# Performance work log

Measured on AMD Instinct MI355X. Metric: run time of the kernel, lower is better.

The kernel has to match this reference:

```python
import jax, jax.numpy as jnp
import numpy as np

N_NODES = 100000
N_EDGES = 600000
HID = 128
N_ETYPES = 8


def setup_inputs() -> dict:
    key = jax.random.key(0)
    ks = jax.random.split(key, 10)
    s = 1.0 / np.sqrt(HID)
    return {
        "h": jax.random.normal(ks[0], (N_NODES, HID), dtype=jnp.float32),
        "edge_index": jax.random.randint(ks[1], (2, N_EDGES), 0, N_NODES, dtype=jnp.int64),
        "edge_type": jax.random.randint(ks[2], (N_EDGES,), 0, N_ETYPES, dtype=jnp.int64),
        # per-edge-type Linear(hidden, hidden): weight (T, H_out, H_in) stored as (T, H_in, H_out) for einsum
        "message_W": jax.random.uniform(ks[3], (N_ETYPES, HID, HID), jnp.float32, -s, s),
        "message_b": jax.random.uniform(ks[4], (N_ETYPES, HID), jnp.float32, -s, s),
        # GRUCell params (torch layout): w_ih (3H, H), w_hh (3H, H), b_ih (3H,), b_hh (3H,)
        "gru_w_ih": jax.random.uniform(ks[5], (3 * HID, HID), jnp.float32, -s, s),
        "gru_w_hh": jax.random.uniform(ks[6], (3 * HID, HID), jnp.float32, -s, s),
        "gru_b_ih": jax.random.uniform(ks[7], (3 * HID,), jnp.float32, -s, s),
        "gru_b_hh": jax.random.uniform(ks[8], (3 * HID,), jnp.float32, -s, s),
    }


def reference(h, edge_index, edge_type, message_W, message_b,
              gru_w_ih, gru_w_hh, gru_b_ih, gru_b_hh):
    num_nodes = h.shape[0]
    src, dst = edge_index[0], edge_index[1]

    # Transform every node by every edge-type Linear once: (N, T, H).
    # Equivalent to per-type msg = h[src] @ W[t].T + b[t] gathered by edge type.
    all_msgs = jnp.einsum('nh,thd->ntd', h, message_W) + message_b  # (N, T, H)
    msg = all_msgs[src, edge_type]                                   # (E, H) gather
    messages = jax.ops.segment_sum(msg, dst, num_segments=num_nodes)  # scatter-add

    # GRUCell: r,z,n gates (torch semantics)
    gi = messages @ gru_w_ih.T + gru_b_ih  # (N, 3H)
    gh = h @ gru_w_hh.T + gru_b_hh         # (N, 3H)
    i_r, i_z, i_n = jnp.split(gi, 3, axis=-1)
    h_r, h_z, h_n = jnp.split(gh, 3, axis=-1)
    r = jax.nn.sigmoid(i_r + h_r)
    z = jax.nn.sigmoid(i_z + h_z)
    n = jnp.tanh(i_n + r * h_n)
    return (1.0 - z) * n + z * h
```

## Files before the change

### kernel.cpp

```cpp
#include <hip/hip_runtime.h>

#define HID 128
#define NTY 8

typedef __attribute__((ext_vector_type(8))) short bf16x8;
typedef __attribute__((ext_vector_type(4))) float f32x4;

__device__ __forceinline__ unsigned short f2bf(float x) {
    unsigned u = __float_as_uint(x);
    u += 0x7FFF + ((u >> 16) & 1);
    return (unsigned short)(u >> 16);
}
__device__ __forceinline__ float bf2f(unsigned short s) {
    return __uint_as_float(((unsigned)s) << 16);
}
__device__ __forceinline__ float sigmoidf_fast(float x) {
    return 1.f / (1.f + __expf(-x));
}
__device__ __forceinline__ float tanhf_fast(float x) {
    return 1.f - 2.f / (1.f + __expf(2.f * x));
}

__global__ void conv_h_kernel(const float* __restrict__ h, unsigned short* __restrict__ hbf, int n) {
    int i = blockIdx.x * 256 + threadIdx.x;
    if (i < n) hbf[i] = f2bf(h[i]);
}
__global__ void conv_W_kernel(const float* __restrict__ W, unsigned short* __restrict__ WbfT) {
    int i = blockIdx.x * 256 + threadIdx.x;
    int t = i >> 14, rem = i & 16383, d = rem >> 7, k = rem & 127;
    WbfT[(t << 14) + (d << 7) + k] = f2bf(W[(t << 14) + (k << 7) + d]);
}
__global__ void conv_wpk_kernel(const float* __restrict__ wih, const float* __restrict__ whh,
                                unsigned short* __restrict__ wpk) {
    int i = blockIdx.x * 256 + threadIdx.x;
    if (i >= 8 * 3 * 128 * 32) return;
    int kk = i & 31;
    int rest = i >> 5;
    int d = rest & 127;
    int rest2 = rest >> 7;
    int g3 = rest2 % 3, kc = rest2 / 3;
    float v;
    if (kc < 4) v = wih[(g3 * 128 + d) * 128 + kc * 32 + kk];
    else        v = whh[(g3 * 128 + d) * 128 + (kc - 4) * 32 + kk];
    wpk[i] = f2bf(v);
}

__global__ void hist_kernel(const int* __restrict__ etype, const int* __restrict__ ei,
                            int E, int* __restrict__ tcnt, int* __restrict__ deg) {
    __shared__ int lc[NTY];
    if (threadIdx.x < NTY) lc[threadIdx.x] = 0;
    __syncthreads();
    int stride = gridDim.x * blockDim.x;
    for (int i = blockIdx.x * blockDim.x + threadIdx.x; i < E; i += stride) {
        atomicAdd(&lc[etype[i]], 1);
        if (deg) atomicAdd(&deg[ei[E + i]], 1);
    }
    __syncthreads();
    if (threadIdx.x < NTY) atomicAdd(&tcnt[threadIdx.x], lc[threadIdx.x]);
}

__global__ void scan_type_kernel(const int* __restrict__ tcnt, int* __restrict__ tcur) {
    if (threadIdx.x == 0) {
        int off = 0;
        for (int t = 0; t < NTY; ++t) { tcur[t] = off; off += (tcnt[t] + 127) & ~127; }
    }
}

__global__ void scanA_kernel(const int* __restrict__ deg, int* __restrict__ start,
                             int* __restrict__ bsum, int N) {
    __shared__ int s[256];
    int i = blockIdx.x * 256 + threadIdx.x;
    int v = (i < N) ? deg[i] : 0;
    s[threadIdx.x] = v;
    __syncthreads();
    for (int off = 1; off < 256; off <<= 1) {
        int t = (threadIdx.x >= off) ? s[threadIdx.x - off] : 0;
        __syncthreads();
        s[threadIdx.x] += t;
        __syncthreads();
    }
    if (i < N) start[i] = s[threadIdx.x] - v;
    if (threadIdx.x == 255) bsum[blockIdx.x] = s[255];
}

__global__ void scanB_kernel(int* __restrict__ bsum, int nb) {
    __shared__ int s[512];
    int tx = threadIdx.x;
    int v = (tx < nb) ? bsum[tx] : 0;
    s[tx] = v;
    __syncthreads();
    for (int off = 1; off < 512; off <<= 1) {
        int t = (tx >= off) ? s[tx - off] : 0;
        __syncthreads();
        s[tx] += t;
        __syncthreads();
    }
    if (tx < nb) bsum[tx] = s[tx] - v;
}

__global__ void scanC_kernel(int* __restrict__ start, const int* __restrict__ bsum,
                             int* __restrict__ dcur, int N, int E) {
    int i = blockIdx.x * 256 + threadIdx.x;
    if (i < N) {
        int v = start[i] + bsum[blockIdx.x];
        start[i] = v;
        dcur[i] = v;
    }
    if (i == 0) start[N] = E;
}

__global__ __launch_bounds__(256) void scatter_agg(
    const int* __restrict__ etype, const int* __restrict__ ei, int E,
    int* __restrict__ tcur, int* __restrict__ dcur,
    int* __restrict__ sortedT, int* __restrict__ q, int mode)
{
    __shared__ int lcnt[NTY];
    __shared__ int lbase[NTY];
    int tx = threadIdx.x;
    int chunk = (E + gridDim.x - 1) / gridDim.x;
    int s = blockIdx.x * chunk;
    int e = s + chunk; if (e > E) e = E;
    if (tx < NTY) lcnt[tx] = 0;
    __syncthreads();
    for (int i = s + tx; i < e; i += 256)
        atomicAdd(&lcnt[etype[i]], 1);
    __syncthreads();
    if (tx < NTY) {
        lbase[tx] = atomicAdd(&tcur[tx], lcnt[tx]);
        lcnt[tx] = 0;
    }
    __syncthreads();
    for (int i = s + tx; i < e; i += 256) {
        int t = etype[i];
        int lp = atomicAdd(&lcnt[t], 1);
        sortedT[lbase[t] + lp] = i;
        if (mode) q[i] = atomicAdd(&dcur[ei[E + i]], 1);
    }
}

__global__ __launch_bounds__(256) void msg_gemm(
    const unsigned short* __restrict__ hbf, const int* __restrict__ ei, int E,
    const int* __restrict__ etype, const unsigned short* __restrict__ WbfT,
    const float* __restrict__ bias, const int* __restrict__ sortedT,
    const int* __restrict__ q, unsigned short* __restrict__ M,
    float* __restrict__ msum, int mode)
{
    __shared__ unsigned short hs[128][136];
    __shared__ unsigned short Bs[128][40];
    __shared__ int srcs[128], aux[128];
    __shared__ int stype;

    int tx = threadIdx.x;
    int base = blockIdx.x * 128;
    if (tx < 128) {
        int id = sortedT[base + tx];
        srcs[tx] = (id >= 0) ? ei[id] : -1;
        aux[tx]  = (id >= 0) ? (mode ? ei[E + id] : q[id]) : -1;
    }
    if (tx == 0) { int id0 = sortedT[base]; stype = (id0 >= 0) ? etype[id0] : -1; }
    __syncthreads();
    int t = stype;
    if (t < 0) return;

    const unsigned short* Wb = WbfT + (t << 14);

    for (int f = tx; f < 2048; f += 256) {
        int row = f >> 4, c8 = (f & 15) * 8;
        int s = srcs[row]; if (s < 0) s = 0;
        *(uint4*)&hs[row][c8] = *(const uint4*)&hbf[(size_t)s * 128 + c8];
    }

    int lane = tx & 63, w = tx >> 6;
    int r0 = (w >> 1) * 64, c0 = (w & 1) * 64;
    int lr = lane & 15, quad = lane >> 4;
    f32x4 acc[4][4] = {};

    for (int kc = 0; kc < 4; ++kc) {
        __syncthreads();
        for (int f = tx; f < 512; f += 256) {
            int d = f >> 2, c8 = (f & 3) * 8;
            *(uint4*)&Bs[d][c8] = *(const uint4*)&Wb[(d << 7) + kc * 32 + c8];
        }
        __syncthreads();
        bf16x8 af[4], bfr[4];
        #pragma unroll
        for (int rb = 0; rb < 4; ++rb) af[rb]  = *(const bf16x8*)&hs[r0 + rb * 16 + lr][kc * 32 + quad * 8];
        #pragma unroll
        for (int cb = 0; cb < 4; ++cb) bfr[cb] = *(const bf16x8*)&Bs[c0 + cb * 16 + lr][quad * 8];
        #pragma unroll
        for (int rb = 0; rb < 4; ++rb)
            #pragma unroll
            for (int cb = 0; cb < 4; ++cb)
                acc[rb][cb] = __builtin_amdgcn_mfma_f32_16x16x32_bf16(bfr[cb], af[rb], acc[rb][cb], 0, 0, 0);
    }

    float4 bv4[4];
    #pragma unroll
    for (int cb = 0; cb < 4; ++cb)
        bv4[cb] = *(const float4*)&bias[t * 128 + c0 + cb * 16 + quad * 4];

    #pragma unroll
    for (int rb = 0; rb < 4; ++rb) {
        int e = r0 + rb * 16 + lr;
        int mr = aux[e];
        if (mr < 0) continue;
        #pragma unroll
        for (int cb = 0; cb < 4; ++cb) {
            int d0 = c0 + cb * 16 + quad * 4;
            f32x4 a = acc[rb][cb];
            if (mode) {
                atomicAdd(&msum[(size_t)mr * 128 + d0 + 0], a[0] + bv4[cb].x);
                atomicAdd(&msum[(size_t)mr * 128 + d0 + 1], a[1] + bv4[cb].y);
                atomicAdd(&msum[(size_t)mr * 128 + d0 + 2], a[2] + bv4[cb].z);
                atomicAdd(&msum[(size_t)mr * 128 + d0 + 3], a[3] + bv4[cb].w);
            } else {
                uint2 v;
                v.x = (unsigned)f2bf(a[0] + bv4[cb].x) | ((unsigned)f2bf(a[1] + bv4[cb].y) << 16);
                v.y = (unsigned)f2bf(a[2] + bv4[cb].z) | ((unsigned)f2bf(a[3] + bv4[cb].w) << 16);
                *(uint2*)&M[(size_t)mr * 128 + d0] = v;
            }
        }
    }
}

__global__ __launch_bounds__(256) void gru_fused(
    const unsigned short* __restrict__ M, const int* __restrict__ start,
    const float* __restrict__ msum_fb, const unsigned short* __restrict__ hbf,
    const unsigned short* __restrict__ wpk, const float* __restrict__ bih,
    const float* __restrict__ bhh, const float* __restrict__ hf,
    float* __restrict__ out, int N, int mode)
{
    __shared__ unsigned short As[64][264];

    int tx = threadIdx.x;
    int n0 = blockIdx.x * 64;

    {
        int node = tx >> 2, qd = tx & 3;
        int n = n0 + node;
        int nc = (n < N) ? n : N - 1;
        float a[32];
        #pragma unroll
        for (int j = 0; j < 32; ++j) a[j] = 0.f;
        if (mode == 0) {
            int s = start[nc], e = start[nc + 1];
            for (int r = s; r < e; ++r) {
                #pragma unroll
                for (int j = 0; j < 4; ++j) {
                    uint4 v = *(const uint4*)&M[(size_t)r * 128 + qd * 32 + j * 8];
                    const unsigned short* pv = (const unsigned short*)&v;
                    #pragma unroll
                    for (int u = 0; u < 8; ++u) a[j * 8 + u] += bf2f(pv[u]);
                }
            }
        } else {
            #pragma unroll
            for (int j = 0; j < 8; ++j) {
                float4 v = *(const float4*)&msum_fb[(size_t)nc * 128 + qd * 32 + j * 4];
                a[j * 4 + 0] = v.x; a[j * 4 + 1] = v.y; a[j * 4 + 2] = v.z; a[j * 4 + 3] = v.w;
            }
        }
        unsigned short tmp[32];
        #pragma unroll
        for (int j = 0; j < 32; ++j) tmp[j] = f2bf(a[j]);
        #pragma unroll
        for (int j = 0; j < 4; ++j)
            *(uint4*)&As[node][qd * 32 + j * 8] = *(const uint4*)&tmp[j * 8];
        #pragma unroll
        for (int j = 0; j < 4; ++j)
            *(uint4*)&As[node][128 + qd * 32 + j * 8] =
                *(const uint4*)&hbf[(size_t)nc * 128 + qd * 32 + j * 8];
    }
    __syncthreads();

    int lane = tx & 63, w = tx >> 6;
    int rt = w & 1, cg = w >> 1;
    int lr = lane & 15, quad = lane >> 4;

    f32x4 aR[4][2] = {}, aZ[4][2] = {}, aI[4][2] = {}, aH[4][2] = {};

    #pragma unroll
    for (int kc = 0; kc < 4; ++kc) {
        bf16x8 af[2];
        #pragma unroll
        for (int r2 = 0; r2 < 2; ++r2)
            af[r2] = *(const bf16x8*)&As[rt * 32 + r2 * 16 + lr][kc * 32 + quad * 8];
        #pragma unroll
        for (int g3 = 0; g3 < 3; ++g3) {
            #pragma unroll
            for (int ct = 0; ct < 4; ++ct) {
                bf16x8 bf = *(const bf16x8*)&wpk[((size_t)((kc * 3 + g3) * 128) + cg * 64 + ct * 16 + lr) * 32 + quad * 8];
                #pragma unroll
                for (int r2 = 0; r2 < 2; ++r2) {
                    if (g3 == 0) aR[ct][r2] = __builtin_amdgcn_mfma_f32_16x16x32_bf16(bf, af[r2], aR[ct][r2], 0, 0, 0);
                    else if (g3 == 1) aZ[ct][r2] = __builtin_amdgcn_mfma_f32_16x16x32_bf16(bf, af[r2], aZ[ct][r2], 0, 0, 0);
                    else aI[ct][r2] = __builtin_amdgcn_mfma_f32_16x16x32_bf16(bf, af[r2], aI[ct][r2], 0, 0, 0);
                }
            }
        }
    }
    #pragma unroll
    for (int kc = 4; kc < 8; ++kc) {
        bf16x8 af[2];
        #pragma unroll
        for (int r2 = 0; r2 < 2; ++r2)
            af[r2] = *(const bf16x8*)&As[rt * 32 + r2 * 16 + lr][kc * 32 + quad * 8];
        #pragma unroll
        for (int g3 = 0; g3 < 3; ++g3) {
            #pragma unroll
            for (int ct = 0; ct < 4; ++ct) {
                bf16x8 bf = *(const bf16x8*)&wpk[((size_t)((kc * 3 + g3) * 128) + cg * 64 + ct * 16 + lr) * 32 + quad * 8];
                #pragma unroll
                for (int r2 = 0; r2 < 2; ++r2) {
                    if (g3 == 0) aR[ct][r2] = __builtin_amdgcn_mfma_f32_16x16x32_bf16(bf, af[r2], aR[ct][r2], 0, 0, 0);
                    else if (g3 == 1) aZ[ct][r2] = __builtin_amdgcn_mfma_f32_16x16x32_bf16(bf, af[r2], aZ[ct][r2], 0, 0, 0);
                    else aH[ct][r2] = __builtin_amdgcn_mfma_f32_16x16x32_bf16(bf, af[r2], aH[ct][r2], 0, 0, 0);
                }
            }
        }
    }

    #pragma unroll
    for (int ct = 0; ct < 4; ++ct) {
        int d0 = cg * 64 + ct * 16 + quad * 4;
        f32x4 bi_r = *(const f32x4*)&bih[d0];
        f32x4 bh_r = *(const f32x4*)&bhh[d0];
        f32x4 bi_z = *(const f32x4*)&bih[128 + d0];
        f32x4 bh_z = *(const f32x4*)&bhh[128 + d0];
        f32x4 bi_n = *(const f32x4*)&bih[256 + d0];
        f32x4 bh_n = *(const f32x4*)&bhh[256 + d0];
        #pragma unroll
        for (int r2 = 0; r2 < 2; ++r2) {
            int n = n0 + rt * 32 + r2 * 16 + lr;
            if (n >= N) continue;
            f32x4 h0 = *(const f32x4*)&hf[(size_t)n * 128 + d0];
            f32x4 o;
            #pragma unroll
            for (int j = 0; j < 4; ++j) {
                float r  = sigmoidf_fast(aR[ct][r2][j] + bi_r[j] + bh_r[j]);
                float z  = sigmoidf_fast(aZ[ct][r2][j] + bi_z[j] + bh_z[j]);
                float nn = tanhf_fast(aI[ct][r2][j] + bi_n[j] + r * (aH[ct][r2][j] + bh_n[j]));
                o[j] = (1.f - z) * nn + z * h0[j];
            }
            *(f32x4*)&out[(size_t)n * 128 + d0] = o;
        }
    }
}

extern "C" void kernel_launch(void* const* d_in, const int* in_sizes, int n_in,
                              void* d_out, int out_size, void* d_ws, size_t ws_size,
                              hipStream_t stream)
{
    const float* h     = (const float*)d_in[0];
    const int*   ei    = (const int*)d_in[1];
    const int*   etype = (const int*)d_in[2];
    const float* W     = (const float*)d_in[3];
    const float* b     = (const float*)d_in[4];
    const float* wih   = (const float*)d_in[5];
    const float* whh   = (const float*)d_in[6];
    const float* bih   = (const float*)d_in[7];
    const float* bhh   = (const float*)d_in[8];
    float* out = (float*)d_out;

    int E = in_sizes[1] / 2;
    int N = in_sizes[0] / HID;
    int capE = ((E + 127) / 128 + NTY) * 128;

    char* p = (char*)d_ws;
    auto alloc = [&](size_t bytes) { char* r = p; p += (bytes + 255) & ~(size_t)255; return r; };
    unsigned short* hbf  = (unsigned short*)alloc((size_t)N * 128 * 2);
    unsigned short* WbfT = (unsigned short*)alloc((size_t)8 * 128 * 128 * 2);
    unsigned short* wpk  = (unsigned short*)alloc((size_t)8 * 3 * 128 * 32 * 2);
    int* tcnt    = (int*)alloc(NTY * 4);
    int* tcur    = (int*)alloc(NTY * 4);
    int* sortedT = (int*)alloc((size_t)capE * 4);
    unsigned short* M = (unsigned short*)alloc((size_t)E * 128 * 2);
    int* q     = (int*)alloc((size_t)E * 4);
    int* deg   = (int*)alloc((size_t)N * 4);
    int* start = (int*)alloc((size_t)(N + 1) * 4);
    int* dcur  = (int*)alloc((size_t)N * 4);
    int* bsum  = (int*)alloc(512 * 4);
    int mode = ((size_t)(p - (char*)d_ws) <= ws_size) ? 0 : 1;

    hipMemsetAsync(tcnt, 0, NTY * 4, stream);
    hipMemsetAsync(sortedT, 0xFF, (size_t)capE * 4, stream);
    if (mode == 0) hipMemsetAsync(deg, 0, (size_t)N * 4, stream);
    else           hipMemsetAsync(out, 0, (size_t)N * 128 * 4, stream);

    conv_h_kernel<<<(N * 128 + 255) / 256, 256, 0, stream>>>(h, hbf, N * 128);
    conv_W_kernel<<<(8 * 128 * 128) / 256, 256, 0, stream>>>(W, WbfT);
    conv_wpk_kernel<<<(8 * 3 * 128 * 32 + 255) / 256, 256, 0, stream>>>(wih, whh, wpk);

    hist_kernel<<<1024, 256, 0, stream>>>(etype, ei, E, tcnt, (mode == 0) ? deg : nullptr);
    scan_type_kernel<<<1, 64, 0, stream>>>(tcnt, tcur);
    if (mode == 0) {
        int nbA = (N + 255) / 256;
        scanA_kernel<<<nbA, 256, 0, stream>>>(deg, start, bsum, N);
        scanB_kernel<<<1, 512, 0, stream>>>(bsum, nbA);
        scanC_kernel<<<nbA, 256, 0, stream>>>(start, bsum, dcur, N, E);
    }
    scatter_agg<<<256, 256, 0, stream>>>(etype, ei, E, tcur, dcur, sortedT, q, (mode == 0) ? 1 : 0);

    msg_gemm<<<capE / 128, 256, 0, stream>>>(hbf, ei, E, etype, WbfT, b, sortedT, q, M, out, mode);
    gru_fused<<<(N + 63) / 64, 256, 0, stream>>>(M, start, out, hbf, wpk, bih, bhh, h, out, N, mode);
}
```

Baseline: 411.7 us.

## Fuse prep kernels, prepack weights in MFMA fragment order, restructure GRU GEMM

Merges the three conversion kernels and the memsets into one launch, and folds the type scan into scanB, cutting launch count. Weights are prepacked in MFMA fragment order, so msg_gemm and gru_fused read B fragments straight from global memory without LDS staging or per-k syncthreads. gru_fused now gives each wave its own 16 nodes, loads h fragments straight into registers, and uses a swizzled per-wave LDS tile. It also splits the work into two output halves to reduce accumulator pressure. The M-row gather loop is software-prefetched one row ahead. The cost is more global and L2 weight traffic per wave and more register use.

```diff
diff --git a/kernel.cpp b/kernel.cpp
--- a/kernel.cpp
+++ b/kernel.cpp
@@ -21,28 +21,44 @@
     return 1.f - 2.f / (1.f + __expf(2.f * x));
 }
 
-__global__ void conv_h_kernel(const float* __restrict__ h, unsigned short* __restrict__ hbf, int n) {
+__global__ void conv_all_kernel(const float* __restrict__ h, unsigned short* __restrict__ hbf, int nh,
+                                const float* __restrict__ W, unsigned short* __restrict__ wfr,
+                                const float* __restrict__ wih, const float* __restrict__ whh,
+                                unsigned short* __restrict__ wpkf,
+                                int* __restrict__ sortedT, int capE,
+                                int* __restrict__ deg, int N, int* __restrict__ tcnt)
+{
     int i = blockIdx.x * 256 + threadIdx.x;
-    if (i < n) hbf[i] = f2bf(h[i]);
-}
-__global__ void conv_W_kernel(const float* __restrict__ W, unsigned short* __restrict__ WbfT) {
-    int i = blockIdx.x * 256 + threadIdx.x;
-    int t = i >> 14, rem = i & 16383, d = rem >> 7, k = rem & 127;
-    WbfT[(t << 14) + (d << 7) + k] = f2bf(W[(t << 14) + (k << 7) + d]);
-}
-__global__ void conv_wpk_kernel(const float* __restrict__ wih, const float* __restrict__ whh,
-                                unsigned short* __restrict__ wpk) {
-    int i = blockIdx.x * 256 + threadIdx.x;
-    if (i >= 8 * 3 * 128 * 32) return;
-    int kk = i & 31;
-    int rest = i >> 5;
-    int d = rest & 127;
-    int rest2 = rest >> 7;
-    int g3 = rest2 % 3, kc = rest2 / 3;
-    float v;
-    if (kc < 4) v = wih[(g3 * 128 + d) * 128 + kc * 32 + kk];
-    else        v = whh[(g3 * 128 + d) * 128 + (kc - 4) * 32 + kk];
-    wpk[i] = f2bf(v);
+    if (i < nh) { hbf[i] = f2bf(h[i]); return; }
+    i -= nh;
+    if (i < 131072) {
+        int e = i & 7, lane = (i >> 3) & 63, cb = (i >> 9) & 7, kc = (i >> 12) & 3, t = i >> 14;
+        int lr = lane & 15, quad = lane >> 4;
+        int d = cb * 16 + lr;
+        int k = kc * 32 + quad * 8 + e;
+        wfr[i] = f2bf(W[(t << 14) + (k << 7) + d]);
+        return;
+    }
+    i -= 131072;
+    if (i < 98304) {
+        int e = i & 7, lane = (i >> 3) & 63, f = i >> 9;
+        int ct = f & 7, fg = f >> 3;
+        int g3 = fg % 3, kc = fg / 3;
+        int lr = lane & 15, quad = lane >> 4;
+        int d = ct * 16 + lr;
+        int kk = quad * 8 + e;
+        float v;
+        if (kc < 4) v = wih[(g3 * 128 + d) * 128 + kc * 32 + kk];
+        else        v = whh[(g3 * 128 + d) * 128 + (kc - 4) * 32 + kk];
+        wpkf[i] = f2bf(v);
+        return;
+    }
+    i -= 98304;
+    if (i < capE) { sortedT[i] = -1; return; }
+    i -= capE;
+    if (i < N) { deg[i] = 0; return; }
+    i -= N;
+    if (i < NTY) tcnt[i] = 0;
 }
 
 __global__ void hist_kernel(const int* __restrict__ etype, const int* __restrict__ ei,
@@ -57,13 +73,6 @@
     }
     __syncthreads();
     if (threadIdx.x < NTY) atomicAdd(&tcnt[threadIdx.x], lc[threadIdx.x]);
-}
-
-__global__ void scan_type_kernel(const int* __restrict__ tcnt, int* __restrict__ tcur) {
-    if (threadIdx.x == 0) {
-        int off = 0;
-        for (int t = 0; t < NTY; ++t) { tcur[t] = off; off += (tcnt[t] + 127) & ~127; }
-    }
 }
 
 __global__ void scanA_kernel(const int* __restrict__ deg, int* __restrict__ start,
@@ -83,7 +92,8 @@
     if (threadIdx.x == 255) bsum[blockIdx.x] = s[255];
 }
 
-__global__ void scanB_kernel(int* __restrict__ bsum, int nb) {
+__global__ void scanB_kernel(int* __restrict__ bsum, int nb,
+                             const int* __restrict__ tcnt, int* __restrict__ tcur) {
     __shared__ int s[512];
     int tx = threadIdx.x;
     int v = (tx < nb) ? bsum[tx] : 0;
@@ -96,6 +106,10 @@
         __syncthreads();
     }
     if (tx < nb) bsum[tx] = s[tx] - v;
+    if (tx == 0) {
+        int off = 0;
+        for (int t = 0; t < NTY; ++t) { tcur[t] = off; off += (tcnt[t] + 127) & ~127; }
+    }
 }
 
 __global__ void scanC_kernel(int* __restrict__ start, const int* __restrict__ bsum,
@@ -140,13 +154,12 @@
 
 __global__ __launch_bounds__(256) void msg_gemm(
     const unsigned short* __restrict__ hbf, const int* __restrict__ ei, int E,
-    const int* __restrict__ etype, const unsigned short* __restrict__ WbfT,
+    const int* __restrict__ etype, const unsigned short* __restrict__ wfr,
     const float* __restrict__ bias, const int* __restrict__ sortedT,
     const int* __restrict__ q, unsigned short* __restrict__ M,
     float* __restrict__ msum, int mode)
 {
     __shared__ unsigned short hs[128][136];
-    __shared__ unsigned short Bs[128][40];
     __shared__ int srcs[128], aux[128];
     __shared__ int stype;
 
@@ -162,36 +175,31 @@
     int t = stype;
     if (t < 0) return;
 
-    const unsigned short* Wb = WbfT + (t << 14);
-
     for (int f = tx; f < 2048; f += 256) {
         int row = f >> 4, c8 = (f & 15) * 8;
         int s = srcs[row]; if (s < 0) s = 0;
         *(uint4*)&hs[row][c8] = *(const uint4*)&hbf[(size_t)s * 128 + c8];
     }
+    __syncthreads();
 
     int lane = tx & 63, w = tx >> 6;
     int r0 = (w >> 1) * 64, c0 = (w & 1) * 64;
     int lr = lane & 15, quad = lane >> 4;
     f32x4 acc[4][4] = {};
 
+    const unsigned short* wt = wfr + (t << 14) + ((unsigned)(c0 >> 4) << 9) + (lane << 3);
+    #pragma unroll
     for (int kc = 0; kc < 4; ++kc) {
-        __syncthreads();
-        for (int f = tx; f < 512; f += 256) {
-            int d = f >> 2, c8 = (f & 3) * 8;
-            *(uint4*)&Bs[d][c8] = *(const uint4*)&Wb[(d << 7) + kc * 32 + c8];
-        }
-        __syncthreads();
-        bf16x8 af[4], bfr[4];
-        #pragma unroll
-        for (int rb = 0; rb < 4; ++rb) af[rb]  = *(const bf16x8*)&hs[r0 + rb * 16 + lr][kc * 32 + quad * 8];
-        #pragma unroll
-        for (int cb = 0; cb < 4; ++cb) bfr[cb] = *(const bf16x8*)&Bs[c0 + cb * 16 + lr][quad * 8];
+        bf16x8 af[4], wf[4];
+        #pragma unroll
+        for (int rb = 0; rb < 4; ++rb) af[rb] = *(const bf16x8*)&hs[r0 + rb * 16 + lr][kc * 32 + quad * 8];
+        #pragma unroll
+        for (int cb = 0; cb < 4; ++cb) wf[cb] = *(const bf16x8*)&wt[(kc << 12) + (cb << 9)];
         #pragma unroll
         for (int rb = 0; rb < 4; ++rb)
             #pragma unroll
             for (int cb = 0; cb < 4; ++cb)
-                acc[rb][cb] = __builtin_amdgcn_mfma_f32_16x16x32_bf16(bfr[cb], af[rb], acc[rb][cb], 0, 0, 0);
+                acc[rb][cb] = __builtin_amdgcn_mfma_f32_16x16x32_bf16(wf[cb], af[rb], acc[rb][cb], 0, 0, 0);
     }
 
     float4 bv4[4];
@@ -226,11 +234,11 @@
 __global__ __launch_bounds__(256) void gru_fused(
     const unsigned short* __restrict__ M, const int* __restrict__ start,
     const float* __restrict__ msum_fb, const unsigned short* __restrict__ hbf,
-    const unsigned short* __restrict__ wpk, const float* __restrict__ bih,
+    const unsigned short* __restrict__ wpkf, const float* __restrict__ bih,
     const float* __restrict__ bhh, const float* __restrict__ hf,
     float* __restrict__ out, int N, int mode)
 {
-    __shared__ unsigned short As[64][264];
+    __shared__ unsigned short As[4][2048];
 
     int tx = threadIdx.x;
     int n0 = blockIdx.x * 64;
@@ -244,13 +252,33 @@
         for (int j = 0; j < 32; ++j) a[j] = 0.f;
         if (mode == 0) {
             int s = start[nc], e = start[nc + 1];
+            uint4 c0v, c1v, c2v, c3v;
+            if (s < e) {
+                const unsigned short* Mp = M + (size_t)s * 128 + qd * 32;
+                c0v = *(const uint4*)(Mp);
+                c1v = *(const uint4*)(Mp + 8);
+                c2v = *(const uint4*)(Mp + 16);
+                c3v = *(const uint4*)(Mp + 24);
+            }
             for (int r = s; r < e; ++r) {
+                uint4 p0 = c0v, p1 = c1v, p2 = c2v, p3 = c3v;
+                if (r + 1 < e) {
+                    const unsigned short* Mn = M + (size_t)(r + 1) * 128 + qd * 32;
+                    c0v = *(const uint4*)(Mn);
+                    c1v = *(const uint4*)(Mn + 8);
+                    c2v = *(const uint4*)(Mn + 16);
+                    c3v = *(const uint4*)(Mn + 24);
+                }
+                const unsigned short* q0 = (const unsigned short*)&p0;
+                const unsigned short* q1 = (const unsigned short*)&p1;
+                const unsigned short* q2 = (const unsigned short*)&p2;
+                const unsigned short* q3 = (const unsigned short*)&p3;
                 #pragma unroll
-                for (int j = 0; j < 4; ++j) {
-                    uint4 v = *(const uint4*)&M[(size_t)r * 128 + qd * 32 + j * 8];
-                    const unsigned short* pv = (const unsigned short*)&v;
-                    #pragma unroll
-                    for (int u = 0; u < 8; ++u) a[j * 8 + u] += bf2f(pv[u]);
+                for (int u = 0; u < 8; ++u) {
+                    a[u]      += bf2f(q0[u]);
+                    a[8 + u]  += bf2f(q1[u]);
+                    a[16 + u] += bf2f(q2[u]);
+                    a[24 + u] += bf2f(q3[u]);
                 }
             }
         } else {
@@ -263,86 +291,93 @@
         unsigned short tmp[32];
         #pragma unroll
         for (int j = 0; j < 32; ++j) tmp[j] = f2bf(a[j]);
-        #pragma unroll
-        for (int j = 0; j < 4; ++j)
-            *(uint4*)&As[node][qd * 32 + j * 8] = *(const uint4*)&tmp[j * 8];
-        #pragma unroll
-        for (int j = 0; j < 4; ++j)
-            *(uint4*)&As[node][128 + qd * 32 + j * 8] =
-                *(const uint4*)&hbf[(size_t)nc * 128 + qd * 32 + j * 8];
+        int lrw = node & 15, wv = node >> 4;
+        #pragma unroll
+        for (int j = 0; j < 4; ++j) {
+            int byte = (lrw << 8) + (qd << 6) + (j << 4);
+            byte ^= (lrw & 7) << 4;
+            *(uint4*)((char*)&As[wv][0] + byte) = *(const uint4*)&tmp[j * 8];
+        }
     }
     __syncthreads();
 
     int lane = tx & 63, w = tx >> 6;
-    int rt = w & 1, cg = w >> 1;
     int lr = lane & 15, quad = lane >> 4;
-
-    f32x4 aR[4][2] = {}, aZ[4][2] = {}, aI[4][2] = {}, aH[4][2] = {};
+    int node = n0 + w * 16 + lr;
+    bool valid = node < N;
+    int nc = valid ? node : (N - 1);
+    unsigned short* AsW = &As[w][0];
+
+    bf16x8 afh[4];
+    {
+        const unsigned short* hrow = hbf + ((size_t)nc << 7) + (quad << 3);
+        #pragma unroll
+        for (int k4 = 0; k4 < 4; ++k4) afh[k4] = *(const bf16x8*)&hrow[k4 * 32];
+    }
+    const unsigned short* wg = wpkf + (lane << 3);
 
     #pragma unroll
-    for (int kc = 0; kc < 4; ++kc) {
-        bf16x8 af[2];
-        #pragma unroll
-        for (int r2 = 0; r2 < 2; ++r2)
-            af[r2] = *(const bf16x8*)&As[rt * 32 + r2 * 16 + lr][kc * 32 + quad * 8];
-        #pragma unroll
-        for (int g3 = 0; g3 < 3; ++g3) {
-            #pragma unroll
-            for (int ct = 0; ct < 4; ++ct) {
-                bf16x8 bf = *(const bf16x8*)&wpk[((size_t)((kc * 3 + g3) * 128) + cg * 64 + ct * 16 + lr) * 32 + quad * 8];
+    for (int dh = 0; dh < 2; ++dh) {
+        f32x4 aR[4] = {}, aZ[4] = {}, aH[4] = {};
+        #pragma unroll
+        for (int kc = 0; kc < 8; ++kc) {
+            bf16x8 af;
+            if (kc < 4) {
+                int byte = ((lr << 8) + (kc << 6) + (quad << 4)) ^ ((lr & 7) << 4);
+                af = *(const bf16x8*)((char*)AsW + byte);
+            } else {
+                af = afh[kc - 4];
+            }
+            #pragma unroll
+            for (int c = 0; c < 4; ++c) {
+                int ct = dh * 4 + c;
+                bf16x8 wfR = *(const bf16x8*)&wg[(unsigned)((kc * 3 + 0) * 8 + ct) << 9];
+                aR[c] = __builtin_amdgcn_mfma_f32_16x16x32_bf16(wfR, af, aR[c], 0, 0, 0);
+                bf16x8 wfZ = *(const bf16x8*)&wg[(unsigned)((kc * 3 + 1) * 8 + ct) << 9];
+                aZ[c] = __builtin_amdgcn_mfma_f32_16x16x32_bf16(wfZ, af, aZ[c], 0, 0, 0);
+                if (kc >= 4) {
+                    bf16x8 wfH = *(const bf16x8*)&wg[(unsigned)((kc * 3 + 2) * 8 + ct) << 9];
+                    aH[c] = __builtin_amdgcn_mfma_f32_16x16x32_bf16(wfH, af, aH[c], 0, 0, 0);
+                }
+            }
+        }
+        f32x4 rv[4], zv[4];
+        #pragma unroll
+        for (int c = 0; c < 4; ++c) {
+            int d0 = (dh * 4 + c) * 16 + quad * 4;
+            f32x4 bir = *(const f32x4*)&bih[d0],       bhr = *(const f32x4*)&bhh[d0];
+            f32x4 biz = *(const f32x4*)&bih[128 + d0], bhz = *(const f32x4*)&bhh[128 + d0];
+            f32x4 bin = *(const f32x4*)&bih[256 + d0], bhn = *(const f32x4*)&bhh[256 + d0];
+            #pragma unroll
+            for (int j = 0; j < 4; ++j) {
+                rv[c][j] = sigmoidf_fast(aR[c][j] + bir[j] + bhr[j]);
+                zv[c][j] = sigmoidf_fast(aZ[c][j] + biz[j] + bhz[j]);
+                aH[c][j] = bin[j] + rv[c][j] * (aH[c][j] + bhn[j]);
+            }
+        }
+        #pragma unroll
+        for (int kc = 0; kc < 4; ++kc) {
+            int byte = ((lr << 8) + (kc << 6) + (quad << 4)) ^ ((lr & 7) << 4);
+            bf16x8 af = *(const bf16x8*)((char*)AsW + byte);
+            #pragma unroll
+            for (int c = 0; c < 4; ++c) {
+                bf16x8 wfH = *(const bf16x8*)&wg[(unsigned)((kc * 3 + 2) * 8 + dh * 4 + c) << 9];
+                aH[c] = __builtin_amdgcn_mfma_f32_16x16x32_bf16(wfH, af, aH[c], 0, 0, 0);
+            }
+        }
+        if (valid) {
+            #pragma unroll
+            for (int c = 0; c < 4; ++c) {
+                int d0 = (dh * 4 + c) * 16 + quad * 4;
+                f32x4 h0 = *(const f32x4*)&hf[(size_t)node * 128 + d0];
+                f32x4 o;
                 #pragma unroll
-                for (int r2 = 0; r2 < 2; ++r2) {
-                    if (g3 == 0) aR[ct][r2] = __builtin_amdgcn_mfma_f32_16x16x32_bf16(bf, af[r2], aR[ct][r2], 0, 0, 0);
-                    else if (g3 == 1) aZ[ct][r2] = __builtin_amdgcn_mfma_f32_16x16x32_bf16(bf, af[r2], aZ[ct][r2], 0, 0, 0);
-                    else aI[ct][r2] = __builtin_amdgcn_mfma_f32_16x16x32_bf16(bf, af[r2], aI[ct][r2], 0, 0, 0);
+                for (int j = 0; j < 4; ++j) {
+                    float nn = tanhf_fast(aH[c][j]);
+                    o[j] = (1.f - zv[c][j]) * nn + zv[c][j] * h0[j];
                 }
-            }
-        }
-    }
-    #pragma unroll
-    for (int kc = 4; kc < 8; ++kc) {
-        bf16x8 af[2];
-        #pragma unroll
-        for (int r2 = 0; r2 < 2; ++r2)
-            af[r2] = *(const bf16x8*)&As[rt * 32 + r2 * 16 + lr][kc * 32 + quad * 8];
-        #pragma unroll
-        for (int g3 = 0; g3 < 3; ++g3) {
-            #pragma unroll
-            for (int ct = 0; ct < 4; ++ct) {
-                bf16x8 bf = *(const bf16x8*)&wpk[((size_t)((kc * 3 + g3) * 128) + cg * 64 + ct * 16 + lr) * 32 + quad * 8];
-                #pragma unroll
-                for (int r2 = 0; r2 < 2; ++r2) {
-                    if (g3 == 0) aR[ct][r2] = __builtin_amdgcn_mfma_f32_16x16x32_bf16(bf, af[r2], aR[ct][r2], 0, 0, 0);
-                    else if (g3 == 1) aZ[ct][r2] = __builtin_amdgcn_mfma_f32_16x16x32_bf16(bf, af[r2], aZ[ct][r2], 0, 0, 0);
-                    else aH[ct][r2] = __builtin_amdgcn_mfma_f32_16x16x32_bf16(bf, af[r2], aH[ct][r2], 0, 0, 0);
-                }
-            }
-        }
-    }
-
-    #pragma unroll
-    for (int ct = 0; ct < 4; ++ct) {
-        int d0 = cg * 64 + ct * 16 + quad * 4;
-        f32x4 bi_r = *(const f32x4*)&bih[d0];
-        f32x4 bh_r = *(const f32x4*)&bhh[d0];
-        f32x4 bi_z = *(const f32x4*)&bih[128 + d0];
-        f32x4 bh_z = *(const f32x4*)&bhh[128 + d0];
-        f32x4 bi_n = *(const f32x4*)&bih[256 + d0];
-        f32x4 bh_n = *(const f32x4*)&bhh[256 + d0];
-        #pragma unroll
-        for (int r2 = 0; r2 < 2; ++r2) {
-            int n = n0 + rt * 32 + r2 * 16 + lr;
-            if (n >= N) continue;
-            f32x4 h0 = *(const f32x4*)&hf[(size_t)n * 128 + d0];
-            f32x4 o;
-            #pragma unroll
-            for (int j = 0; j < 4; ++j) {
-                float r  = sigmoidf_fast(aR[ct][r2][j] + bi_r[j] + bh_r[j]);
-                float z  = sigmoidf_fast(aZ[ct][r2][j] + bi_z[j] + bh_z[j]);
-                float nn = tanhf_fast(aI[ct][r2][j] + bi_n[j] + r * (aH[ct][r2][j] + bh_n[j]));
-                o[j] = (1.f - z) * nn + z * h0[j];
-            }
-            *(f32x4*)&out[(size_t)n * 128 + d0] = o;
+                *(f32x4*)&out[(size_t)node * 128 + d0] = o;
+            }
         }
     }
 }
@@ -365,12 +400,13 @@
     int E = in_sizes[1] / 2;
     int N = in_sizes[0] / HID;
     int capE = ((E + 127) / 128 + NTY) * 128;
+    int nbA = (N + 255) / 256;
 
     char* p = (char*)d_ws;
     auto alloc = [&](size_t bytes) { char* r = p; p += (bytes + 255) & ~(size_t)255; return r; };
     unsigned short* hbf  = (unsigned short*)alloc((size_t)N * 128 * 2);
-    unsigned short* WbfT = (unsigned short*)alloc((size_t)8 * 128 * 128 * 2);
-    unsigned short* wpk  = (unsigned short*)alloc((size_t)8 * 3 * 128 * 32 * 2);
+    unsigned short* wfr  = (unsigned short*)alloc((size_t)131072 * 2);
+    unsigned short* wpkf = (unsigned short*)alloc((size_t)98304 * 2);
     int* tcnt    = (int*)alloc(NTY * 4);
     int* tcur    = (int*)alloc(NTY * 4);
     int* sortedT = (int*)alloc((size_t)capE * 4);
@@ -382,25 +418,20 @@
     int* bsum  = (int*)alloc(512 * 4);
     int mode = ((size_t)(p - (char*)d_ws) <= ws_size) ? 0 : 1;
 
-    hipMemsetAsync(tcnt, 0, NTY * 4, stream);
-    hipMemsetAsync(sortedT, 0xFF, (size_t)capE * 4, stream);
-    if (mode == 0) hipMemsetAsync(deg, 0, (size_t)N * 4, stream);
-    else           hipMemsetAsync(out, 0, (size_t)N * 128 * 4, stream);
-
-    conv_h_kernel<<<(N * 128 + 255) / 256, 256, 0, stream>>>(h, hbf, N * 128);
-    conv_W_kernel<<<(8 * 128 * 128) / 256, 256, 0, stream>>>(W, WbfT);
-    conv_wpk_kernel<<<(8 * 3 * 128 * 32 + 255) / 256, 256, 0, stream>>>(wih, whh, wpk);
+    if (mode == 1) hipMemsetAsync(out, 0, (size_t)N * 128 * 4, stream);
+
+    int totalConv = N * 128 + 131072 + 98304 + capE + N + NTY;
+    conv_all_kernel<<<(totalConv + 255) / 256, 256, 0, stream>>>(
+        h, hbf, N * 128, W, wfr, wih, whh, wpkf, sortedT, capE, deg, N, tcnt);
 
     hist_kernel<<<1024, 256, 0, stream>>>(etype, ei, E, tcnt, (mode == 0) ? deg : nullptr);
-    scan_type_kernel<<<1, 64, 0, stream>>>(tcnt, tcur);
-    if (mode == 0) {
-        int nbA = (N + 255) / 256;
+    if (mode == 0)
         scanA_kernel<<<nbA, 256, 0, stream>>>(deg, start, bsum, N);
-        scanB_kernel<<<1, 512, 0, stream>>>(bsum, nbA);
+    scanB_kernel<<<1, 512, 0, stream>>>(bsum, nbA, tcnt, tcur);
+    if (mode == 0)
         scanC_kernel<<<nbA, 256, 0, stream>>>(start, bsum, dcur, N, E);
-    }
     scatter_agg<<<256, 256, 0, stream>>>(etype, ei, E, tcur, dcur, sortedT, q, (mode == 0) ? 1 : 0);
 
-    msg_gemm<<<capE / 128, 256, 0, stream>>>(hbf, ei, E, etype, WbfT, b, sortedT, q, M, out, mode);
-    gru_fused<<<(N + 63) / 64, 256, 0, stream>>>(M, start, out, hbf, wpk, bih, bhh, h, out, N, mode);
-}
+    msg_gemm<<<capE / 128, 256, 0, stream>>>(hbf, ei, E, etype, wfr, b, sortedT, q, M, out, mode);
+    gru_fused<<<(N + 63) / 64, 256, 0, stream>>>(M, start, out, hbf, wpkf, bih, bhh, h, out, N, mode);
+}
```

Result: no change. 404.5 us (-1.8%).
